# Kernel tuning notes

Measured on AMD Instinct MI355X. Metric: run time of the kernel, lower is better.

## Reference

```python
import jax, jax.numpy as jnp
import numpy as np
import math

B, S, H = 2, 2048, 768
NH, HD = 12, 64  # num_sparse_heads, attention_head_size
VOCAB = 30522


def setup_inputs() -> dict:
    key = jax.random.key(0)
    ks = jax.random.split(key, 6)
    scale = 0.02
    return {
        "hidden_states": jax.random.normal(ks[0], (B, S, H), dtype=jnp.float32),
        "attention_mask": jnp.zeros((B, S), dtype=jnp.float32),
        "input_ids": jax.random.randint(ks[1], (B, S), 0, VOCAB, dtype=jnp.int64) if jax.config.read('jax_enable_x64') else jax.random.randint(ks[1], (B, S), 0, VOCAB, dtype=jnp.int32),
        "ngram": 1,
        "Wq": jax.random.normal(ks[2], (H, H), dtype=jnp.float32) * scale,
        "bq": jnp.zeros((H,), dtype=jnp.float32),
        "Wk": jax.random.normal(ks[3], (H, H), dtype=jnp.float32) * scale,
        "bk": jnp.zeros((H,), dtype=jnp.float32),
    }


def reference(hidden_states, attention_mask, input_ids, ngram, Wq, bq, Wk, bk):
    # Linear projections (torch Linear: x @ W.T + b)
    q = hidden_states @ Wq.T + bq  # [B, S, H]
    k = hidden_states @ Wk.T + bk  # [B, S, H]
    # split heads -> [B, NH, S, HD]
    q = q.reshape(B, S, NH, HD).transpose(0, 2, 1, 3)
    k = k.reshape(B, S, NH, HD).transpose(0, 2, 1, 3)
    # QK^T scores, scale, additive mask over the QUERY axis (mask[:, None, :, None]), ReLU
    scores = jnp.einsum('bhqd,bhkd->bhqk', q, k) / math.sqrt(HD)
    scores = scores + attention_mask[:, None, :, None]
    probs = jax.nn.relu(scores)
    # context_layer = probs.transpose(1, 2) -> [B, S, NH, S]
    return jnp.swapaxes(probs, 1, 2)
```

## Files before the change

kernel.cpp:

```cpp
#include <hip/hip_runtime.h>
#include <hip/hip_bf16.h>
#include <stdint.h>

#define Bb  2
#define Ss  2048
#define Hh  768
#define NHh 12
#define HDd 64

typedef short bf16x8 __attribute__((ext_vector_type(8)));
typedef float f32x4  __attribute__((ext_vector_type(4)));
typedef unsigned short u16x4 __attribute__((ext_vector_type(4)));

__device__ __forceinline__ unsigned short f2bf(float x) {
    union { float f; unsigned int u; } v; v.f = x;
    unsigned int r = v.u + 0x7fffu + ((v.u >> 16) & 1u);
    return (unsigned short)(r >> 16);
}

__device__ __forceinline__ void gl_lds16(const unsigned short* g, unsigned short* l) {
    __builtin_amdgcn_global_load_lds(
        (const __attribute__((address_space(1))) unsigned int*)g,
        (__attribute__((address_space(3))) unsigned int*)l, 16, 0, 0);
}

__global__ __launch_bounds__(256)
void cast_kernel(const float* __restrict__ hs, const float* __restrict__ Wq,
                 const float* __restrict__ Wk,
                 unsigned short* __restrict__ hsb, unsigned short* __restrict__ Wqb,
                 unsigned short* __restrict__ Wkb)
{
    int cid = blockIdx.x * 256 + threadIdx.x;
    const float* src; unsigned short* dst; int base;
    if (cid < 393216)      { src = hs; dst = hsb; base = cid; }
    else if (cid < 466944) { src = Wq; dst = Wqb; base = cid - 393216; }
    else                   { src = Wk; dst = Wkb; base = cid - 466944; }
    float4 a0 = ((const float4*)src)[(size_t)base * 2];
    float4 a1 = ((const float4*)src)[(size_t)base * 2 + 1];
    bf16x8 v;
    v[0] = (short)f2bf(a0.x); v[1] = (short)f2bf(a0.y);
    v[2] = (short)f2bf(a0.z); v[3] = (short)f2bf(a0.w);
    v[4] = (short)f2bf(a1.x); v[5] = (short)f2bf(a1.y);
    v[6] = (short)f2bf(a1.z); v[7] = (short)f2bf(a1.w);
    ((bf16x8*)dst)[base] = v;
}

__global__ __launch_bounds__(256)
void proj_kernel(const unsigned short* __restrict__ hsb,
                 const unsigned short* __restrict__ Wqb,
                 const unsigned short* __restrict__ Wkb,
                 const float* __restrict__ bq, const float* __restrict__ bk,
                 unsigned short* __restrict__ Qb, unsigned short* __restrict__ Kb)
{
    const int zq = blockIdx.z;
    const unsigned short* __restrict__ Wb = zq ? Wkb : Wqb;
    const float* __restrict__ bias = zq ? bk : bq;
    unsigned short* __restrict__ Out = zq ? Kb : Qb;

    const int m0 = blockIdx.x * 128;
    const int n0 = blockIdx.y * 128;

    __shared__ unsigned short As[128 * 64];
    __shared__ unsigned short Bs[128 * 64];

    const int tid  = threadIdx.x;
    const int lane = tid & 63;
    const int w    = tid >> 6;
    const int wm   = (w >> 1) * 64;
    const int wn   = (w & 1) * 64;
    const int lg   = lane >> 4;
    const int l15  = lane & 15;

    f32x4 acc[4][4] = {};

    for (int k0 = 0; k0 < Hh; k0 += 64) {
        #pragma unroll
        for (int i = 0; i < 4; ++i) {
            int cc  = i * 256 + tid;
            int row = cc >> 3, seg = (cc & 7) * 8;
            gl_lds16(hsb + (size_t)(m0 + row) * Hh + k0 + seg, &As[cc * 8]);
            gl_lds16(Wb  + (size_t)(n0 + row) * Hh + k0 + seg, &Bs[cc * 8]);
        }
        __syncthreads();

        #pragma unroll
        for (int kk = 0; kk < 2; ++kk) {
            const int kof = kk * 32 + lg * 8;
            bf16x8 wf[4], hf[4];
            #pragma unroll
            for (int i = 0; i < 4; ++i)
                wf[i] = *(bf16x8*)&Bs[(wm + i * 16 + l15) * 64 + kof];
            #pragma unroll
            for (int j = 0; j < 4; ++j)
                hf[j] = *(bf16x8*)&As[(wn + j * 16 + l15) * 64 + kof];
            #pragma unroll
            for (int i = 0; i < 4; ++i)
                #pragma unroll
                for (int j = 0; j < 4; ++j)
                    acc[i][j] = __builtin_amdgcn_mfma_f32_16x16x32_bf16(
                        wf[i], hf[j], acc[i][j], 0, 0, 0);
        }
        __syncthreads();
    }

    #pragma unroll
    for (int i = 0; i < 4; ++i) {
        const int nb = n0 + wm + i * 16 + lg * 4;
        const float4 bv = *(const float4*)&bias[nb];
        #pragma unroll
        for (int j = 0; j < 4; ++j) {
            const int m = m0 + wn + j * 16 + l15;
            u16x4 o;
            o[0] = f2bf(acc[i][j][0] + bv.x);
            o[1] = f2bf(acc[i][j][1] + bv.y);
            o[2] = f2bf(acc[i][j][2] + bv.z);
            o[3] = f2bf(acc[i][j][3] + bv.w);
            *(u16x4*)&Out[(size_t)m * Hh + nb] = o;
        }
    }
}

__global__ __launch_bounds__(256)
void score_kernel(const unsigned short* __restrict__ Qb,
                  const unsigned short* __restrict__ Kb,
                  const float* __restrict__ mask,
                  float* __restrict__ out)
{
    const int q0 = blockIdx.x * 128;
    const int c0 = blockIdx.y * 128;
    const int bh = blockIdx.z;
    const int b  = bh / NHh, h = bh % NHh;

    __shared__ unsigned short Qs[128 * 64];
    __shared__ unsigned short Ks[128 * 64];

    const int tid  = threadIdx.x;
    const int lane = tid & 63;
    const int w    = tid >> 6;
    const int wm   = (w >> 1) * 64;
    const int wn   = (w & 1) * 64;
    const int lg   = lane >> 4;
    const int l15  = lane & 15;

    #pragma unroll
    for (int i = 0; i < 4; ++i) {
        int cc  = i * 256 + tid;
        int row = cc >> 3, seg = (cc & 7) * 8;
        gl_lds16(Qb + (size_t)(b * Ss + q0 + row) * Hh + h * HDd + seg, &Qs[cc * 8]);
        gl_lds16(Kb + (size_t)(b * Ss + c0 + row) * Hh + h * HDd + seg, &Ks[cc * 8]);
    }
    __syncthreads();

    f32x4 acc[4][4] = {};
    #pragma unroll
    for (int kk = 0; kk < 2; ++kk) {
        const int kof = kk * 32 + lg * 8;
        bf16x8 kf[4], qf[4];
        #pragma unroll
        for (int m = 0; m < 4; ++m)
            kf[m] = *(bf16x8*)&Ks[(wm + m * 16 + l15) * 64 + kof];
        #pragma unroll
        for (int n = 0; n < 4; ++n)
            qf[n] = *(bf16x8*)&Qs[(wn + n * 16 + l15) * 64 + kof];
        #pragma unroll
        for (int m = 0; m < 4; ++m)
            #pragma unroll
            for (int n = 0; n < 4; ++n)
                acc[m][n] = __builtin_amdgcn_mfma_f32_16x16x32_bf16(
                    kf[m], qf[n], acc[m][n], 0, 0, 0);
    }

    #pragma unroll
    for (int n = 0; n < 4; ++n) {
        const int q = q0 + wn + n * 16 + l15;
        const float mv = mask[b * Ss + q];
        float* orow = out + ((size_t)(b * Ss + q) * NHh + h) * Ss;
        #pragma unroll
        for (int m = 0; m < 4; ++m) {
            const int kb = c0 + wm + m * 16 + lg * 4;
            float4 o;
            float v0 = acc[m][n][0] * 0.125f + mv;
            float v1 = acc[m][n][1] * 0.125f + mv;
            float v2 = acc[m][n][2] * 0.125f + mv;
            float v3 = acc[m][n][3] * 0.125f + mv;
            o.x = v0 > 0.f ? v0 : 0.f;
            o.y = v1 > 0.f ? v1 : 0.f;
            o.z = v2 > 0.f ? v2 : 0.f;
            o.w = v3 > 0.f ? v3 : 0.f;
            *(float4*)&orow[kb] = o;
        }
    }
}

extern "C" void kernel_launch(void* const* d_in, const int* in_sizes, int n_in,
                              void* d_out, int out_size, void* d_ws, size_t ws_size,
                              hipStream_t stream) {
    const float* hs   = (const float*)d_in[0];
    const float* mask = (const float*)d_in[1];
    const float* Wq = (const float*)d_in[4];
    const float* bq = (const float*)d_in[5];
    const float* Wk = (const float*)d_in[6];
    const float* bk = (const float*)d_in[7];
    float* out = (float*)d_out;

    unsigned short* Qb  = (unsigned short*)d_ws;
    unsigned short* Kb  = Qb  + 3145728;
    unsigned short* hsb = Kb  + 3145728;
    unsigned short* Wqb = hsb + 3145728;
    unsigned short* Wkb = Wqb + 589824;

    cast_kernel<<<2112, 256, 0, stream>>>(hs, Wq, Wk, hsb, Wqb, Wkb);
    proj_kernel<<<dim3(32, 6, 2), 256, 0, stream>>>(hsb, Wqb, Wkb, bq, bk, Qb, Kb);
    score_kernel<<<dim3(16, 16, 24), 256, 0, stream>>>(Qb, Kb, mask, out);
}
```

Baseline: 118.0 us.

## Swizzle LDS tiles, shrink projection M tile, remap score blocks across XCDs

Applies an XOR swizzle to the LDS layout of all GEMM tiles so fragment reads avoid bank conflicts. Halves the projection kernel's M tile to 64 to double its block count and fill more CUs. Replaces the 3D score grid with a 1D grid whose block index is remapped so consecutive blocks spread across the eight XCDs. Together these target LDS bank conflicts, projection under-occupancy and cache locality in the score kernel, which is dominated by its large fp32 output write.

```diff
diff --git a/kernel.cpp b/kernel.cpp
--- a/kernel.cpp
+++ b/kernel.cpp
@@ -22,6 +22,10 @@
     __builtin_amdgcn_global_load_lds(
         (const __attribute__((address_space(1))) unsigned int*)g,
         (__attribute__((address_space(3))) unsigned int*)l, 16, 0, 0);
+}
+
+__device__ __forceinline__ bf16x8 ldfrag(const unsigned short* lds, int row, int s) {
+    return *(const bf16x8*)&lds[(row << 6) + ((s ^ (row & 7)) << 3)];
 }
 
 __global__ __launch_bounds__(256)
@@ -57,11 +61,88 @@
     const float* __restrict__ bias = zq ? bk : bq;
     unsigned short* __restrict__ Out = zq ? Kb : Qb;
 
-    const int m0 = blockIdx.x * 128;
+    const int m0 = blockIdx.x * 64;
     const int n0 = blockIdx.y * 128;
 
-    __shared__ unsigned short As[128 * 64];
+    __shared__ unsigned short As[64 * 64];
     __shared__ unsigned short Bs[128 * 64];
+
+    const int tid  = threadIdx.x;
+    const int lane = tid & 63;
+    const int w    = tid >> 6;
+    const int wc   = (w & 1) * 64;
+    const int wr   = (w >> 1) * 32;
+    const int lg   = lane >> 4;
+    const int l15  = lane & 15;
+
+    f32x4 acc[4][2] = {};
+
+    for (int k0 = 0; k0 < Hh; k0 += 64) {
+        #pragma unroll
+        for (int i = 0; i < 2; ++i) {
+            int cc = i * 256 + tid, row = cc >> 3, seg = cc & 7;
+            gl_lds16(hsb + (size_t)(m0 + row) * Hh + k0 + ((seg ^ (row & 7)) << 3),
+                     &As[cc * 8]);
+        }
+        #pragma unroll
+        for (int i = 0; i < 4; ++i) {
+            int cc = i * 256 + tid, row = cc >> 3, seg = cc & 7;
+            gl_lds16(Wb + (size_t)(n0 + row) * Hh + k0 + ((seg ^ (row & 7)) << 3),
+                     &Bs[cc * 8]);
+        }
+        __syncthreads();
+
+        #pragma unroll
+        for (int kk = 0; kk < 2; ++kk) {
+            const int s = kk * 4 + lg;
+            bf16x8 wf[4], hf[2];
+            #pragma unroll
+            for (int i = 0; i < 4; ++i) wf[i] = ldfrag(Bs, wc + i * 16 + l15, s);
+            #pragma unroll
+            for (int j = 0; j < 2; ++j) hf[j] = ldfrag(As, wr + j * 16 + l15, s);
+            #pragma unroll
+            for (int i = 0; i < 4; ++i)
+                #pragma unroll
+                for (int j = 0; j < 2; ++j)
+                    acc[i][j] = __builtin_amdgcn_mfma_f32_16x16x32_bf16(
+                        wf[i], hf[j], acc[i][j], 0, 0, 0);
+        }
+        __syncthreads();
+    }
+
+    #pragma unroll
+    for (int i = 0; i < 4; ++i) {
+        const int nb = n0 + wc + i * 16 + lg * 4;
+        const float4 bv = *(const float4*)&bias[nb];
+        #pragma unroll
+        for (int j = 0; j < 2; ++j) {
+            const int m = m0 + wr + j * 16 + l15;
+            u16x4 o;
+            o[0] = f2bf(acc[i][j][0] + bv.x);
+            o[1] = f2bf(acc[i][j][1] + bv.y);
+            o[2] = f2bf(acc[i][j][2] + bv.z);
+            o[3] = f2bf(acc[i][j][3] + bv.w);
+            *(u16x4*)&Out[(size_t)m * Hh + nb] = o;
+        }
+    }
+}
+
+__global__ __launch_bounds__(256)
+void score_kernel(const unsigned short* __restrict__ Qb,
+                  const unsigned short* __restrict__ Kb,
+                  const float* __restrict__ mask,
+                  float* __restrict__ out)
+{
+    const int bid = blockIdx.x;
+    const int gid = (bid & 7) * 768 + (bid >> 3);
+    const int bh  = gid >> 8;
+    const int rem = gid & 255;
+    const int c0  = (rem >> 4) * 128;
+    const int q0  = (rem & 15) * 128;
+    const int b   = bh / NHh, h = bh % NHh;
+
+    __shared__ unsigned short Qs[128 * 64];
+    __shared__ unsigned short Ks[128 * 64];
 
     const int tid  = threadIdx.x;
     const int lane = tid & 63;
@@ -71,97 +152,24 @@
     const int lg   = lane >> 4;
     const int l15  = lane & 15;
 
+    #pragma unroll
+    for (int i = 0; i < 4; ++i) {
+        int cc = i * 256 + tid, row = cc >> 3, seg = cc & 7;
+        const int sg = (seg ^ (row & 7)) << 3;
+        gl_lds16(Qb + (size_t)(b * Ss + q0 + row) * Hh + h * HDd + sg, &Qs[cc * 8]);
+        gl_lds16(Kb + (size_t)(b * Ss + c0 + row) * Hh + h * HDd + sg, &Ks[cc * 8]);
+    }
+    __syncthreads();
+
     f32x4 acc[4][4] = {};
-
-    for (int k0 = 0; k0 < Hh; k0 += 64) {
-        #pragma unroll
-        for (int i = 0; i < 4; ++i) {
-            int cc  = i * 256 + tid;
-            int row = cc >> 3, seg = (cc & 7) * 8;
-            gl_lds16(hsb + (size_t)(m0 + row) * Hh + k0 + seg, &As[cc * 8]);
-            gl_lds16(Wb  + (size_t)(n0 + row) * Hh + k0 + seg, &Bs[cc * 8]);
-        }
-        __syncthreads();
-
-        #pragma unroll
-        for (int kk = 0; kk < 2; ++kk) {
-            const int kof = kk * 32 + lg * 8;
-            bf16x8 wf[4], hf[4];
-            #pragma unroll
-            for (int i = 0; i < 4; ++i)
-                wf[i] = *(bf16x8*)&Bs[(wm + i * 16 + l15) * 64 + kof];
-            #pragma unroll
-            for (int j = 0; j < 4; ++j)
-                hf[j] = *(bf16x8*)&As[(wn + j * 16 + l15) * 64 + kof];
-            #pragma unroll
-            for (int i = 0; i < 4; ++i)
-                #pragma unroll
-                for (int j = 0; j < 4; ++j)
-                    acc[i][j] = __builtin_amdgcn_mfma_f32_16x16x32_bf16(
-                        wf[i], hf[j], acc[i][j], 0, 0, 0);
-        }
-        __syncthreads();
-    }
-
-    #pragma unroll
-    for (int i = 0; i < 4; ++i) {
-        const int nb = n0 + wm + i * 16 + lg * 4;
-        const float4 bv = *(const float4*)&bias[nb];
-        #pragma unroll
-        for (int j = 0; j < 4; ++j) {
-            const int m = m0 + wn + j * 16 + l15;
-            u16x4 o;
-            o[0] = f2bf(acc[i][j][0] + bv.x);
-            o[1] = f2bf(acc[i][j][1] + bv.y);
-            o[2] = f2bf(acc[i][j][2] + bv.z);
-            o[3] = f2bf(acc[i][j][3] + bv.w);
-            *(u16x4*)&Out[(size_t)m * Hh + nb] = o;
-        }
-    }
-}
-
-__global__ __launch_bounds__(256)
-void score_kernel(const unsigned short* __restrict__ Qb,
-                  const unsigned short* __restrict__ Kb,
-                  const float* __restrict__ mask,
-                  float* __restrict__ out)
-{
-    const int q0 = blockIdx.x * 128;
-    const int c0 = blockIdx.y * 128;
-    const int bh = blockIdx.z;
-    const int b  = bh / NHh, h = bh % NHh;
-
-    __shared__ unsigned short Qs[128 * 64];
-    __shared__ unsigned short Ks[128 * 64];
-
-    const int tid  = threadIdx.x;
-    const int lane = tid & 63;
-    const int w    = tid >> 6;
-    const int wm   = (w >> 1) * 64;
-    const int wn   = (w & 1) * 64;
-    const int lg   = lane >> 4;
-    const int l15  = lane & 15;
-
-    #pragma unroll
-    for (int i = 0; i < 4; ++i) {
-        int cc  = i * 256 + tid;
-        int row = cc >> 3, seg = (cc & 7) * 8;
-        gl_lds16(Qb + (size_t)(b * Ss + q0 + row) * Hh + h * HDd + seg, &Qs[cc * 8]);
-        gl_lds16(Kb + (size_t)(b * Ss + c0 + row) * Hh + h * HDd + seg, &Ks[cc * 8]);
-    }
-    __syncthreads();
-
-    f32x4 acc[4][4] = {};
     #pragma unroll
     for (int kk = 0; kk < 2; ++kk) {
-        const int kof = kk * 32 + lg * 8;
+        const int s = kk * 4 + lg;
         bf16x8 kf[4], qf[4];
         #pragma unroll
-        for (int m = 0; m < 4; ++m)
-            kf[m] = *(bf16x8*)&Ks[(wm + m * 16 + l15) * 64 + kof];
-        #pragma unroll
-        for (int n = 0; n < 4; ++n)
-            qf[n] = *(bf16x8*)&Qs[(wn + n * 16 + l15) * 64 + kof];
+        for (int m = 0; m < 4; ++m) kf[m] = ldfrag(Ks, wm + m * 16 + l15, s);
+        #pragma unroll
+        for (int n = 0; n < 4; ++n) qf[n] = ldfrag(Qs, wn + n * 16 + l15, s);
         #pragma unroll
         for (int m = 0; m < 4; ++m)
             #pragma unroll
@@ -210,6 +218,6 @@
     unsigned short* Wkb = Wqb + 589824;
 
     cast_kernel<<<2112, 256, 0, stream>>>(hs, Wq, Wk, hsb, Wqb, Wkb);
-    proj_kernel<<<dim3(32, 6, 2), 256, 0, stream>>>(hsb, Wqb, Wkb, bq, bk, Qb, Kb);
-    score_kernel<<<dim3(16, 16, 24), 256, 0, stream>>>(Qb, Kb, mask, out);
-}
+    proj_kernel<<<dim3(64, 6, 2), 256, 0, stream>>>(hsb, Wqb, Wkb, bq, bk, Qb, Kb);
+    score_kernel<<<6144, 256, 0, stream>>>(Qb, Kb, mask, out);
+}
```

Measured after the change: 133.8 us. +13.4%, slower.
